# Kernel tuning notes

Hardware: AMD Instinct MI355X
Metric: run time of the kernel (lower is better)

## Reference

```python
import jax, jax.numpy as jnp
import numpy as np

IN_F = 4096
OUT_F = 16384
TOKENS = 64


def setup_inputs() -> dict:
    key = jax.random.key(0)
    k1, k2, k3 = jax.random.split(key, 3)
    x = jax.random.normal(k1, (TOKENS, IN_F), dtype=jnp.float16)
    # int8-valued weights stored as int32 (same math after cast to fp16)
    weight = jax.random.randint(k2, (OUT_F, IN_F), -127, 127, dtype=jnp.int32)
    weight_scales = jax.random.uniform(k3, (OUT_F,), dtype=jnp.float16, minval=0.001, maxval=0.02)
    bias = jnp.zeros((1, OUT_F), dtype=jnp.float16)
    return {"x": x, "weight": weight, "weight_scales": weight_scales, "bias": bias}


def reference(x, weight, weight_scales, bias):
    # Dequantize int8 weight to fp16 with per-output-channel scale, then linear.
    w_fp16 = weight.astype(jnp.float16) * weight_scales[:, None]  # [out, in]
    y = jnp.dot(x, w_fp16.T) + bias  # [tokens, out]
    return y
```

## Files before the change

kernel.cpp:

```cpp
#include <hip/hip_runtime.h>
#include <hip/hip_bf16.h>
#include <hip/hip_fp16.h>

#define IN_F 4096
#define OUT_F 16384
#define TOKENS 64
#define NWAVE 8
#define KCHUNK (IN_F / NWAVE)
#define BLOCK (NWAVE * 64)

typedef __attribute__((ext_vector_type(8))) short bf16x8;
typedef __attribute__((ext_vector_type(8))) unsigned short u16x8;
typedef __attribute__((ext_vector_type(4))) float f32x4;
typedef __attribute__((ext_vector_type(4))) int i32x4;

enum { F_BF16 = 0, F_FP16 = 1, F_FP32 = 2 };

__device__ __forceinline__ float dec_bf16(unsigned short h) {
    return __uint_as_float(((unsigned)h) << 16);
}
__device__ __forceinline__ float dec_fp16(unsigned short h) {
    __half_raw hr; hr.x = h;
    return __half2float(__half(hr));
}
__device__ __forceinline__ unsigned short enc_bf16_rne(float f) {
    unsigned u = __float_as_uint(f);
    u += 0x7FFFu + ((u >> 16) & 1u);
    return (unsigned short)(u >> 16);
}

__device__ __forceinline__ int detect_fmt16(const void* p, int lane, float lo, float hi) {
    unsigned short h = ((const unsigned short*)p)[lane];
    float vb = fabsf(dec_bf16(h));
    float vh = fabsf(dec_fp16(h));
    int cb = __popcll(__ballot(vb > lo && vb < hi));
    int ch = __popcll(__ballot(vh > lo && vh < hi));
    return (cb >= 56) ? F_BF16 : (ch >= 56) ? F_FP16 : F_FP32;
}
__device__ __forceinline__ int detect_wint(const int* w, int lane) {
    int v = w[lane];
    int ci = __popcll(__ballot(v >= -127 && v <= 127));
    return (ci >= 56) ? 1 : 0;
}

template <int XF, int WINT>
__device__ __forceinline__ void kloop(const void* xv, const void* wv,
                                      size_t wrow, int kbase, int kq, int ln,
                                      f32x4 acc[4]) {
    #pragma unroll 4
    for (int k0 = 0; k0 < KCHUNK; k0 += 32) {
        const int kk = kbase + k0 + kq * 8;

        bf16x8 bfrag;
        if (WINT) {
            const int* wp = (const int*)wv + wrow + kk;
            i32x4 b0 = *(const i32x4*)(wp);
            i32x4 b1 = *(const i32x4*)(wp + 4);
            #pragma unroll
            for (int j = 0; j < 4; ++j) {
                bfrag[j]     = (short)(__float_as_uint((float)b0[j]) >> 16);
                bfrag[j + 4] = (short)(__float_as_uint((float)b1[j]) >> 16);
            }
        } else {
            const float* wp = (const float*)wv + wrow + kk;
            f32x4 b0 = *(const f32x4*)(wp);
            f32x4 b1 = *(const f32x4*)(wp + 4);
            #pragma unroll
            for (int j = 0; j < 4; ++j) {
                bfrag[j]     = (short)(__float_as_uint(b0[j]) >> 16);
                bfrag[j + 4] = (short)(__float_as_uint(b1[j]) >> 16);
            }
        }

        bf16x8 afrag[4];
        #pragma unroll
        for (int t = 0; t < 4; ++t) {
            const size_t row = (size_t)(ln + 16 * t) * IN_F;
            if (XF == F_BF16) {
                afrag[t] = *(const bf16x8*)((const short*)xv + row + kk);
            } else if (XF == F_FP32) {
                const float* xp = (const float*)xv + row + kk;
                f32x4 a0 = *(const f32x4*)xp;
                f32x4 a1 = *(const f32x4*)(xp + 4);
                #pragma unroll
                for (int j = 0; j < 4; ++j) {
                    afrag[t][j]     = (short)enc_bf16_rne(a0[j]);
                    afrag[t][j + 4] = (short)enc_bf16_rne(a1[j]);
                }
            } else {
                u16x8 a = *(const u16x8*)((const unsigned short*)xv + row + kk);
                #pragma unroll
                for (int j = 0; j < 8; ++j)
                    afrag[t][j] = (short)enc_bf16_rne(dec_fp16(a[j]));
            }
        }

        acc[0] = __builtin_amdgcn_mfma_f32_16x16x32_bf16(afrag[0], bfrag, acc[0], 0, 0, 0);
        acc[1] = __builtin_amdgcn_mfma_f32_16x16x32_bf16(afrag[1], bfrag, acc[1], 0, 0, 0);
        acc[2] = __builtin_amdgcn_mfma_f32_16x16x32_bf16(afrag[2], bfrag, acc[2], 0, 0, 0);
        acc[3] = __builtin_amdgcn_mfma_f32_16x16x32_bf16(afrag[3], bfrag, acc[3], 0, 0, 0);
    }
}

__global__ __launch_bounds__(BLOCK) void w8a16_main(const void* __restrict__ xv,
                                                    const void* __restrict__ wv,
                                                    const void* __restrict__ sv,
                                                    const void* __restrict__ bv,
                                                    void* __restrict__ yv) {
    __shared__ float red[NWAVE][64][17];

    const int tid  = threadIdx.x;
    const int wave = tid >> 6;
    const int lane = tid & 63;
    const int ln   = lane & 15;
    const int kq   = lane >> 4;

    const int xf = detect_fmt16(xv, lane, 9.7e-4f, 64.0f);
    const int sf = detect_fmt16(sv, lane, 1.0e-4f, 0.25f);
    const int wi = detect_wint((const int*)wv, lane);

    const int    n     = blockIdx.x * 16 + ln;
    const size_t wrow  = (size_t)n * IN_F;
    const int    kbase = wave * KCHUNK;

    f32x4 acc[4] = {};

    if (wi) {
        if (xf == F_BF16)      kloop<F_BF16, 1>(xv, wv, wrow, kbase, kq, ln, acc);
        else if (xf == F_FP32) kloop<F_FP32, 1>(xv, wv, wrow, kbase, kq, ln, acc);
        else                   kloop<F_FP16, 1>(xv, wv, wrow, kbase, kq, ln, acc);
    } else {
        if (xf == F_BF16)      kloop<F_BF16, 0>(xv, wv, wrow, kbase, kq, ln, acc);
        else if (xf == F_FP32) kloop<F_FP32, 0>(xv, wv, wrow, kbase, kq, ln, acc);
        else                   kloop<F_FP16, 0>(xv, wv, wrow, kbase, kq, ln, acc);
    }

    #pragma unroll
    for (int i = 0; i < 4; ++i)
        #pragma unroll
        for (int r = 0; r < 4; ++r)
            red[wave][lane][i * 4 + r] = acc[i][r];
    __syncthreads();

    #pragma unroll
    for (int e0 = 0; e0 < TOKENS * 16; e0 += BLOCK) {
        const int e    = e0 + tid;
        const int nl   = e & 15;
        const int m    = e >> 4;
        const int i    = m >> 4;
        const int ml   = m & 15;
        const int lsrc = (ml >> 2) * 16 + nl;
        const int aidx = i * 4 + (ml & 3);

        float s = 0.f;
        #pragma unroll
        for (int wv2 = 0; wv2 < NWAVE; ++wv2) s += red[wv2][lsrc][aidx];

        const int ng = blockIdx.x * 16 + nl;
        float scale, bias;
        if (sf == F_FP32) {
            scale = ((const float*)sv)[ng];
            bias  = ((const float*)bv)[ng];
        } else if (sf == F_BF16) {
            scale = dec_bf16(((const unsigned short*)sv)[ng]);
            bias  = dec_bf16(((const unsigned short*)bv)[ng]);
        } else {
            scale = dec_fp16(((const unsigned short*)sv)[ng]);
            bias  = dec_fp16(((const unsigned short*)bv)[ng]);
        }

        const float  val  = s * scale + bias;
        const size_t oidx = (size_t)m * OUT_F + ng;
        if (xf == F_FP32)      ((float*)yv)[oidx] = val;
        else if (xf == F_BF16) ((unsigned short*)yv)[oidx] = enc_bf16_rne(val);
        else                   ((__half*)yv)[oidx] = __float2half(val);
    }
}

extern "C" void kernel_launch(void* const* d_in, const int* in_sizes, int n_in,
                              void* d_out, int out_size, void* d_ws, size_t ws_size,
                              hipStream_t stream) {
    w8a16_main<<<OUT_F / 16, BLOCK, 0, stream>>>(d_in[0], d_in[1], d_in[2], d_in[3], d_out);
}
```

Baseline: 456.3 us.

## Stage weight tiles via async global-to-LDS double buffering with x prepass

Adds a prepass kernel that converts x to bf16 once into workspace, so the main loop no longer reconverts activations per block. The main kernel now handles 32 output rows per 256-thread block, split across two K halves. Weight tiles are streamed into swizzled, double-buffered LDS with global_load_lds so loads overlap MFMA work, and a two-way LDS reduction replaces the eight-way one. The aim is to improve bandwidth use on the 256MB int32 weight stream, at the cost of an extra launch and more barriers per tile.

Result: faster. 381.0 us (-16.5%).

```diff
diff --git a/kernel.cpp b/kernel.cpp
--- a/kernel.cpp
+++ b/kernel.cpp
@@ -5,9 +5,13 @@
 #define IN_F 4096
 #define OUT_F 16384
 #define TOKENS 64
-#define NWAVE 8
-#define KCHUNK (IN_F / NWAVE)
-#define BLOCK (NWAVE * 64)
+
+#define NT 32
+#define KT 128
+#define KHALF 2048
+#define NTILES 16
+#define TILE_BYTES (NT * KT * 4)
+#define BLOCK 256
 
 typedef __attribute__((ext_vector_type(8))) short bf16x8;
 typedef __attribute__((ext_vector_type(8))) unsigned short u16x8;
@@ -43,142 +47,175 @@
     return (ci >= 56) ? 1 : 0;
 }
 
-template <int XF, int WINT>
-__device__ __forceinline__ void kloop(const void* xv, const void* wv,
-                                      size_t wrow, int kbase, int kq, int ln,
-                                      f32x4 acc[4]) {
-    #pragma unroll 4
-    for (int k0 = 0; k0 < KCHUNK; k0 += 32) {
-        const int kk = kbase + k0 + kq * 8;
-
+__global__ __launch_bounds__(256) void prep_x(const void* __restrict__ xv,
+                                              unsigned short* __restrict__ xbf) {
+    const int tid  = blockIdx.x * 256 + threadIdx.x;
+    const int lane = threadIdx.x & 63;
+    const int xf = detect_fmt16(xv, lane, 9.7e-4f, 64.0f);
+
+    if (xf == F_BF16) {
+        u16x8 a = ((const u16x8*)xv)[tid * 2];
+        u16x8 b = ((const u16x8*)xv)[tid * 2 + 1];
+        ((u16x8*)xbf)[tid * 2]     = a;
+        ((u16x8*)xbf)[tid * 2 + 1] = b;
+    } else if (xf == F_FP32) {
+        u16x8 o[2];
+        #pragma unroll
+        for (int half = 0; half < 2; ++half) {
+            f32x4 v0 = ((const f32x4*)xv)[tid * 4 + half * 2];
+            f32x4 v1 = ((const f32x4*)xv)[tid * 4 + half * 2 + 1];
+            #pragma unroll
+            for (int j = 0; j < 4; ++j) {
+                o[half][j]     = enc_bf16_rne(v0[j]);
+                o[half][j + 4] = enc_bf16_rne(v1[j]);
+            }
+        }
+        ((u16x8*)xbf)[tid * 2]     = o[0];
+        ((u16x8*)xbf)[tid * 2 + 1] = o[1];
+    } else {
+        #pragma unroll
+        for (int half = 0; half < 2; ++half) {
+            u16x8 v = ((const u16x8*)xv)[tid * 2 + half];
+            u16x8 o;
+            #pragma unroll
+            for (int j = 0; j < 8; ++j) o[j] = enc_bf16_rne(dec_fp16(v[j]));
+            ((u16x8*)xbf)[tid * 2 + half] = o;
+        }
+    }
+}
+
+template <int WINT>
+__device__ __forceinline__ void tile_compute(const char* __restrict__ buf,
+                                             const unsigned short* __restrict__ xbf,
+                                             int kbase, int ln, int kq, int row,
+                                             f32x4 acc[4]) {
+    const char*  bufb = buf + row * 512;
+    const short* xs   = (const short*)xbf;
+    #pragma unroll
+    for (int kt = 0; kt < 4; ++kt) {
+        const int c0 = kt * 8 + 2 * kq;
+        i32x4 b0 = *(const i32x4*)(bufb + ((c0)     ^ ln) * 16);
+        i32x4 b1 = *(const i32x4*)(bufb + ((c0 + 1) ^ ln) * 16);
         bf16x8 bfrag;
-        if (WINT) {
-            const int* wp = (const int*)wv + wrow + kk;
-            i32x4 b0 = *(const i32x4*)(wp);
-            i32x4 b1 = *(const i32x4*)(wp + 4);
-            #pragma unroll
-            for (int j = 0; j < 4; ++j) {
-                bfrag[j]     = (short)(__float_as_uint((float)b0[j]) >> 16);
-                bfrag[j + 4] = (short)(__float_as_uint((float)b1[j]) >> 16);
-            }
-        } else {
-            const float* wp = (const float*)wv + wrow + kk;
-            f32x4 b0 = *(const f32x4*)(wp);
-            f32x4 b1 = *(const f32x4*)(wp + 4);
-            #pragma unroll
-            for (int j = 0; j < 4; ++j) {
-                bfrag[j]     = (short)(__float_as_uint(b0[j]) >> 16);
-                bfrag[j + 4] = (short)(__float_as_uint(b1[j]) >> 16);
-            }
-        }
-
-        bf16x8 afrag[4];
-        #pragma unroll
-        for (int t = 0; t < 4; ++t) {
-            const size_t row = (size_t)(ln + 16 * t) * IN_F;
-            if (XF == F_BF16) {
-                afrag[t] = *(const bf16x8*)((const short*)xv + row + kk);
-            } else if (XF == F_FP32) {
-                const float* xp = (const float*)xv + row + kk;
-                f32x4 a0 = *(const f32x4*)xp;
-                f32x4 a1 = *(const f32x4*)(xp + 4);
-                #pragma unroll
-                for (int j = 0; j < 4; ++j) {
-                    afrag[t][j]     = (short)enc_bf16_rne(a0[j]);
-                    afrag[t][j + 4] = (short)enc_bf16_rne(a1[j]);
-                }
-            } else {
-                u16x8 a = *(const u16x8*)((const unsigned short*)xv + row + kk);
-                #pragma unroll
-                for (int j = 0; j < 8; ++j)
-                    afrag[t][j] = (short)enc_bf16_rne(dec_fp16(a[j]));
-            }
-        }
-
-        acc[0] = __builtin_amdgcn_mfma_f32_16x16x32_bf16(afrag[0], bfrag, acc[0], 0, 0, 0);
-        acc[1] = __builtin_amdgcn_mfma_f32_16x16x32_bf16(afrag[1], bfrag, acc[1], 0, 0, 0);
-        acc[2] = __builtin_amdgcn_mfma_f32_16x16x32_bf16(afrag[2], bfrag, acc[2], 0, 0, 0);
-        acc[3] = __builtin_amdgcn_mfma_f32_16x16x32_bf16(afrag[3], bfrag, acc[3], 0, 0, 0);
-    }
-}
-
-__global__ __launch_bounds__(BLOCK) void w8a16_main(const void* __restrict__ xv,
-                                                    const void* __restrict__ wv,
-                                                    const void* __restrict__ sv,
-                                                    const void* __restrict__ bv,
-                                                    void* __restrict__ yv) {
-    __shared__ float red[NWAVE][64][17];
+        #pragma unroll
+        for (int j = 0; j < 4; ++j) {
+            unsigned f0 = WINT ? __float_as_uint((float)b0[j]) : (unsigned)b0[j];
+            unsigned f1 = WINT ? __float_as_uint((float)b1[j]) : (unsigned)b1[j];
+            bfrag[j]     = (short)(f0 >> 16);
+            bfrag[j + 4] = (short)(f1 >> 16);
+        }
+        const int kk = kbase + kt * 32 + kq * 8;
+        bf16x8 a0 = *(const bf16x8*)(xs + (size_t)(ln     ) * IN_F + kk);
+        bf16x8 a1 = *(const bf16x8*)(xs + (size_t)(ln + 16) * IN_F + kk);
+        bf16x8 a2 = *(const bf16x8*)(xs + (size_t)(ln + 32) * IN_F + kk);
+        bf16x8 a3 = *(const bf16x8*)(xs + (size_t)(ln + 48) * IN_F + kk);
+        acc[0] = __builtin_amdgcn_mfma_f32_16x16x32_bf16(a0, bfrag, acc[0], 0, 0, 0);
+        acc[1] = __builtin_amdgcn_mfma_f32_16x16x32_bf16(a1, bfrag, acc[1], 0, 0, 0);
+        acc[2] = __builtin_amdgcn_mfma_f32_16x16x32_bf16(a2, bfrag, acc[2], 0, 0, 0);
+        acc[3] = __builtin_amdgcn_mfma_f32_16x16x32_bf16(a3, bfrag, acc[3], 0, 0, 0);
+    }
+}
+
+__global__ __launch_bounds__(BLOCK, 2) void w8a16_main(
+    const void* __restrict__ xv_orig, const int* __restrict__ w,
+    const void* __restrict__ sv, const void* __restrict__ bv,
+    void* __restrict__ yv, const unsigned short* __restrict__ xbf) {
+
+    __shared__ alignas(16) char lds[2][2][TILE_BYTES];
 
     const int tid  = threadIdx.x;
-    const int wave = tid >> 6;
+    const int wv   = tid >> 6;
     const int lane = tid & 63;
     const int ln   = lane & 15;
     const int kq   = lane >> 4;
-
-    const int xf = detect_fmt16(xv, lane, 9.7e-4f, 64.0f);
+    const int h    = wv >> 1;
+    const int wl   = wv & 1;
+    const int n0   = blockIdx.x * NT;
+
+    const int xf = detect_fmt16(xv_orig, lane, 9.7e-4f, 64.0f);
     const int sf = detect_fmt16(sv, lane, 1.0e-4f, 0.25f);
-    const int wi = detect_wint((const int*)wv, lane);
-
-    const int    n     = blockIdx.x * 16 + ln;
-    const size_t wrow  = (size_t)n * IN_F;
-    const int    kbase = wave * KCHUNK;
+    const int wi = detect_wint(w, lane);
+
+    const int th   = tid >> 7;
+    const int t127 = tid & 127;
+    auto stage = [&](int tile, int dbuf) {
+        #pragma unroll
+        for (int j = 0; j < 8; ++j) {
+            const int idx = j * 128 + t127;
+            const int r   = idx >> 5;
+            const int c   = idx & 31;
+            const int cg  = c ^ (r & 15);
+            const int* g = w + (size_t)(n0 + r) * IN_F + th * KHALF + tile * KT + cg * 4;
+            char* l = &lds[th][dbuf][idx * 16];
+            __builtin_amdgcn_global_load_lds(
+                (const __attribute__((address_space(1))) unsigned int*)g,
+                (__attribute__((address_space(3))) unsigned int*)l, 16, 0, 0);
+        }
+    };
 
     f32x4 acc[4] = {};
-
-    if (wi) {
-        if (xf == F_BF16)      kloop<F_BF16, 1>(xv, wv, wrow, kbase, kq, ln, acc);
-        else if (xf == F_FP32) kloop<F_FP32, 1>(xv, wv, wrow, kbase, kq, ln, acc);
-        else                   kloop<F_FP16, 1>(xv, wv, wrow, kbase, kq, ln, acc);
-    } else {
-        if (xf == F_BF16)      kloop<F_BF16, 0>(xv, wv, wrow, kbase, kq, ln, acc);
-        else if (xf == F_FP32) kloop<F_FP32, 0>(xv, wv, wrow, kbase, kq, ln, acc);
-        else                   kloop<F_FP16, 0>(xv, wv, wrow, kbase, kq, ln, acc);
-    }
-
-    #pragma unroll
-    for (int i = 0; i < 4; ++i)
-        #pragma unroll
-        for (int r = 0; r < 4; ++r)
-            red[wave][lane][i * 4 + r] = acc[i][r];
+    const int row = 16 * wl + ln;
+
+    stage(0, 0);
     __syncthreads();
-
-    #pragma unroll
-    for (int e0 = 0; e0 < TOKENS * 16; e0 += BLOCK) {
-        const int e    = e0 + tid;
-        const int nl   = e & 15;
-        const int m    = e >> 4;
-        const int i    = m >> 4;
-        const int ml   = m & 15;
-        const int lsrc = (ml >> 2) * 16 + nl;
-        const int aidx = i * 4 + (ml & 3);
-
-        float s = 0.f;
-        #pragma unroll
-        for (int wv2 = 0; wv2 < NWAVE; ++wv2) s += red[wv2][lsrc][aidx];
-
-        const int ng = blockIdx.x * 16 + nl;
+    for (int t = 0; t < NTILES; ++t) {
+        if (t + 1 < NTILES) stage(t + 1, (t + 1) & 1);
+        const char* buf   = &lds[h][t & 1][0];
+        const int   kbase = h * KHALF + t * KT;
+        if (wi) tile_compute<1>(buf, xbf, kbase, ln, kq, row, acc);
+        else    tile_compute<0>(buf, xbf, kbase, ln, kq, row, acc);
+        __syncthreads();
+    }
+
+    float* red = (float*)&lds[0][0][0];
+    if (h == 1) {
+        #pragma unroll
+        for (int i = 0; i < 4; ++i)
+            #pragma unroll
+            for (int r2 = 0; r2 < 4; ++r2)
+                red[(wl * 64 + lane) * 16 + i * 4 + r2] = acc[i][r2];
+    }
+    __syncthreads();
+    if (h == 0) {
+        #pragma unroll
+        for (int i = 0; i < 4; ++i)
+            #pragma unroll
+            for (int r2 = 0; r2 < 4; ++r2)
+                acc[i][r2] += red[(wl * 64 + lane) * 16 + i * 4 + r2];
+
+        const int n = n0 + row;
         float scale, bias;
         if (sf == F_FP32) {
-            scale = ((const float*)sv)[ng];
-            bias  = ((const float*)bv)[ng];
+            scale = ((const float*)sv)[n];
+            bias  = ((const float*)bv)[n];
         } else if (sf == F_BF16) {
-            scale = dec_bf16(((const unsigned short*)sv)[ng]);
-            bias  = dec_bf16(((const unsigned short*)bv)[ng]);
+            scale = dec_bf16(((const unsigned short*)sv)[n]);
+            bias  = dec_bf16(((const unsigned short*)bv)[n]);
         } else {
-            scale = dec_fp16(((const unsigned short*)sv)[ng]);
-            bias  = dec_fp16(((const unsigned short*)bv)[ng]);
-        }
-
-        const float  val  = s * scale + bias;
-        const size_t oidx = (size_t)m * OUT_F + ng;
-        if (xf == F_FP32)      ((float*)yv)[oidx] = val;
-        else if (xf == F_BF16) ((unsigned short*)yv)[oidx] = enc_bf16_rne(val);
-        else                   ((__half*)yv)[oidx] = __float2half(val);
+            scale = dec_fp16(((const unsigned short*)sv)[n]);
+            bias  = dec_fp16(((const unsigned short*)bv)[n]);
+        }
+
+        #pragma unroll
+        for (int i = 0; i < 4; ++i) {
+            #pragma unroll
+            for (int r2 = 0; r2 < 4; ++r2) {
+                const int    m   = 16 * i + kq * 4 + r2;
+                const float  val = acc[i][r2] * scale + bias;
+                const size_t o   = (size_t)m * OUT_F + n;
+                if (xf == F_FP32)      ((float*)yv)[o] = val;
+                else if (xf == F_BF16) ((unsigned short*)yv)[o] = enc_bf16_rne(val);
+                else                   ((__half*)yv)[o] = __float2half(val);
+            }
+        }
     }
 }
 
 extern "C" void kernel_launch(void* const* d_in, const int* in_sizes, int n_in,
                               void* d_out, int out_size, void* d_ws, size_t ws_size,
                               hipStream_t stream) {
-    w8a16_main<<<OUT_F / 16, BLOCK, 0, stream>>>(d_in[0], d_in[1], d_in[2], d_in[3], d_out);
-}
+    unsigned short* xbf = (unsigned short*)d_ws;
+    prep_x<<<64, 256, 0, stream>>>(d_in[0], xbf);
+    w8a16_main<<<OUT_F / NT, BLOCK, 0, stream>>>(d_in[0], (const int*)d_in[1],
+                                                 d_in[2], d_in[3], d_out, xbf);
+}
```
